# Performance work log

Hardware: AMD Instinct MI355X
Metric: run time of the kernel (lower is better)

The kernel has to match this reference:

```python
import jax, jax.numpy as jnp
import numpy as np

N_NODES = 100000


def _gcn_conv(x, W, b, src, dst, num_nodes):
    # x: [N, Fin] -> h: [N, Fout]
    h = x @ W
    # symmetric normalization deg^-1/2[src] * deg^-1/2[dst] (self-loops already appended)
    ones = jnp.ones(src.shape[0], dtype=x.dtype)
    deg = jax.ops.segment_sum(ones, dst, num_segments=num_nodes)
    dinv = jnp.where(deg > 0, jax.lax.rsqrt(deg), 0.0)
    norm = dinv[src] * dinv[dst]  # [E]
    msg = h[src] * norm[:, None]  # [E, Fout] -- dominant memory traffic
    out = jax.ops.segment_sum(msg, dst, num_segments=num_nodes)
    return out + b


def setup_inputs() -> dict:
    key = jax.random.key(0)
    ks = jax.random.split(key, 8)
    N, F_IN, H = N_NODES, 128, 64
    E = 3200000
    x = jax.random.normal(ks[0], (N, F_IN), dtype=jnp.float32)
    edge_index = jax.random.randint(ks[1], (2, E), 0, N, dtype=jnp.int64)
    s1 = 1.0 / np.sqrt(F_IN)
    s2 = 1.0 / np.sqrt(H)
    return {
        "x": x,
        "edge_index": edge_index,
        "W1": jax.random.normal(ks[2], (F_IN, H), dtype=jnp.float32) * s1,
        "b1": jnp.zeros((H,), dtype=jnp.float32),
        "W2": jax.random.normal(ks[3], (H, H), dtype=jnp.float32) * s2,
        "b2": jnp.zeros((H,), dtype=jnp.float32),
        "W_time": jax.random.normal(ks[4], (H, 1), dtype=jnp.float32) * s2,
        "b_time": jnp.zeros((1,), dtype=jnp.float32),
        "W_event": jax.random.normal(ks[5], (H, 1), dtype=jnp.float32) * s2,
        "b_event": jnp.zeros((1,), dtype=jnp.float32),
    }


def reference(x, edge_index, W1, b1, W2, b2, W_time, b_time, W_event, b_event):
    N = x.shape[0]
    # GCNConv default: add self-loops before normalization/aggregation
    loops = jnp.arange(N, dtype=edge_index.dtype)
    src = jnp.concatenate([edge_index[0], loops])
    dst = jnp.concatenate([edge_index[1], loops])

    h = jax.nn.relu(_gcn_conv(x, W1, b1, src, dst, N))
    # dropout is identity in eval mode
    h = jax.nn.relu(_gcn_conv(h, W2, b2, src, dst, N))

    survival_time = h @ W_time + b_time    # [N, 1]
    event_status = h @ W_event + b_event   # [N, 1]
    return survival_time, event_status
```

## Files before the change

kernel.cpp:

```cpp
#include <hip/hip_runtime.h>
#include <math.h>

constexpr int H = 64;
constexpr int FIN = 128;
constexpr int BIN_SHIFT = 8;
constexpr int BIN_NODES = 1 << BIN_SHIFT;
constexpr int MAX_BINS = 512;
constexpr int BIN_CAP = 10240;
constexpr int SRC_BITS = 24;
constexpr unsigned SRC_MASK = (1u << SRC_BITS) - 1;
constexpr int KB_BLOCKS = 512;
constexpr int KB_ITER = 25;

typedef __attribute__((ext_vector_type(8))) __bf16 bf16x8;
typedef __attribute__((ext_vector_type(4))) float f32x4;

__device__ inline float bf2f(unsigned short u) {
    unsigned v = ((unsigned)u) << 16;
    return __builtin_bit_cast(float, v);
}
__device__ inline unsigned short f2bf(float f) {
    unsigned u = __builtin_bit_cast(unsigned, f);
    unsigned rnd = 0x7FFFu + ((u >> 16) & 1u);
    return (unsigned short)((u + rnd) >> 16);
}

__device__ inline int wave_incl_scan(int v, int lane) {
#pragma unroll
    for (int off = 1; off < 64; off <<= 1) {
        int t = __shfl_up(v, off);
        if (lane >= off) v += t;
    }
    return v;
}

__global__ void k_initcur(int* __restrict__ cursor, int nbins) {
    int i = blockIdx.x * blockDim.x + threadIdx.x;
    if (i < nbins) cursor[i] = i * BIN_CAP;
}

__global__ __launch_bounds__(256) void k_bin(
    const int* __restrict__ src, const int* __restrict__ dst, int E, int nbins,
    int* __restrict__ cursor, int* __restrict__ binned) {
    __shared__ int hist[MAX_BINS];
    __shared__ int base[MAX_BINS];
    int tid = threadIdx.x;
    long long e0 = (long long)E * blockIdx.x / gridDim.x;
    long long e1 = (long long)E * (blockIdx.x + 1) / gridDim.x;
    int chunk = (int)(e1 - e0);
    for (int i = tid; i < nbins; i += 256) hist[i] = 0;
    __syncthreads();
    int packed[KB_ITER];
#pragma unroll
    for (int i = 0; i < KB_ITER; ++i) {
        int o = i * 256 + tid;
        packed[i] = -1;
        if (o < chunk) {
            int d = dst[e0 + o];
            int b = d >> BIN_SHIFT;
            int r = atomicAdd(&hist[b], 1);
            packed[i] = (b << 22) | ((d & (BIN_NODES - 1)) << 14) | r;
        }
    }
    __syncthreads();
    for (int i = tid; i < nbins; i += 256) {
        int h = hist[i];
        base[i] = h ? atomicAdd(&cursor[i], h) : 0;
    }
    __syncthreads();
#pragma unroll
    for (int i = 0; i < KB_ITER; ++i) {
        int o = i * 256 + tid;
        if (o < chunk) {
            unsigned w = (unsigned)packed[i];
            int b = (int)(w >> 22);
            int dl = (int)((w >> 14) & 0xFF);
            int r = (int)(w & 0x3FFF);
            binned[base[b] + r] = (int)(((unsigned)dl << SRC_BITS) | (unsigned)src[e0 + o]);
        }
    }
    for (int o = KB_ITER * 256 + tid; o < chunk; o += 256) {
        int d = dst[e0 + o];
        int b = d >> BIN_SHIFT;
        int r = atomicAdd(&cursor[b], 1);
        binned[r] = (int)(((unsigned)(d & (BIN_NODES - 1)) << SRC_BITS) | (unsigned)src[e0 + o]);
    }
}

__global__ __launch_bounds__(256) void k_binscan(
    const int* __restrict__ cursor, int nbins,
    int* __restrict__ binbase, int* __restrict__ rowptr, int N, int E) {
    __shared__ int wsum[4];
    int tid = threadIdx.x, lane = tid & 63, wid = tid >> 6;
    int b0 = tid * 4;
    int c[4];
#pragma unroll
    for (int k = 0; k < 4; ++k) {
        int b = b0 + k;
        c[k] = (b < nbins) ? cursor[b] - b * BIN_CAP : 0;
    }
    int t = c[0] + c[1] + c[2] + c[3];
    int incl = wave_incl_scan(t, lane);
    if (lane == 63) wsum[wid] = incl;
    __syncthreads();
    int woff = 0;
    for (int w = 0; w < wid; ++w) woff += wsum[w];
    int p = woff + incl - t;
#pragma unroll
    for (int k = 0; k < 4; ++k) {
        int b = b0 + k;
        if (b < nbins) binbase[b] = p;
        p += c[k];
    }
    if (tid == 0) rowptr[N] = E;
}

__global__ __launch_bounds__(256) void k_binsort(
    const int* __restrict__ cursor, const int* __restrict__ binbase,
    const int* __restrict__ binned, int N,
    int* __restrict__ csr_src, int* __restrict__ rowptr, float* __restrict__ dinv) {
    __shared__ int cnt[BIN_NODES];
    __shared__ int excl[BIN_NODES];
    __shared__ int rnk[BIN_NODES];
    __shared__ int wsum[4];
    int bin = blockIdx.x;
    int tid = threadIdx.x, lane = tid & 63, wid = tid >> 6;
    int n = cursor[bin] - bin * BIN_CAP;
    int gbase = binbase[bin];
    const int* bp = binned + (size_t)bin * BIN_CAP;
    cnt[tid] = 0; rnk[tid] = 0;
    __syncthreads();
    for (int i = tid; i < n; i += 256)
        atomicAdd(&cnt[((unsigned)bp[i]) >> SRC_BITS], 1);
    __syncthreads();
    int v = cnt[tid];
    int incl = wave_incl_scan(v, lane);
    if (lane == 63) wsum[wid] = incl;
    __syncthreads();
    int woff = 0;
    for (int w = 0; w < wid; ++w) woff += wsum[w];
    int ex = woff + incl - v;
    excl[tid] = ex;
    int node = bin * BIN_NODES + tid;
    if (node < N) {
        rowptr[node] = gbase + ex;
        dinv[node] = 1.0f / sqrtf((float)v + 1.0f);
    }
    __syncthreads();
    for (int i = tid; i < n; i += 256) {
        unsigned w = (unsigned)bp[i];
        int dl = w >> SRC_BITS;
        int r = atomicAdd(&rnk[dl], 1);
        csr_src[gbase + excl[dl] + r] = (int)(w & SRC_MASK);
    }
}

template<int K, bool RELU_IN>
__global__ __launch_bounds__(256) void k_mgemm(
    const float* __restrict__ X, const float* __restrict__ W,
    const float* __restrict__ bias, const float* __restrict__ dinv,
    int N, unsigned short* __restrict__ A16) {
    constexpr int LDK = K + 8;
    __shared__ short sX[64 * LDK];
    __shared__ short sWt[64 * LDK];
    int tid = threadIdx.x;
    for (int idx = tid; idx < K * 64; idx += 256) {
        int k = idx >> 6, c = idx & 63;
        sWt[c * LDK + k] = (short)f2bf(W[idx]);
    }
    {
        int row = tid >> 2;
        int q0 = (tid & 3) * (K / 4);
        int grow = blockIdx.x * 64 + row;
        const float* xp = X + (size_t)grow * K + q0;
        unsigned* dstp = (unsigned*)&sX[row * LDK + q0];
#pragma unroll
        for (int i = 0; i < K / 16; ++i) {
            float4 v = make_float4(0.f, 0.f, 0.f, 0.f);
            if (grow < N) v = *(const float4*)(xp + i * 4);
            if (RELU_IN) {
                float4 bb = *(const float4*)(bias + q0 + i * 4);
                v.x = fmaxf(v.x + bb.x, 0.f); v.y = fmaxf(v.y + bb.y, 0.f);
                v.z = fmaxf(v.z + bb.z, 0.f); v.w = fmaxf(v.w + bb.w, 0.f);
            }
            unsigned lo = (unsigned)f2bf(v.x) | ((unsigned)f2bf(v.y) << 16);
            unsigned hi = (unsigned)f2bf(v.z) | ((unsigned)f2bf(v.w) << 16);
            dstp[i * 2] = lo;
            dstp[i * 2 + 1] = hi;
        }
    }
    __syncthreads();
    int w = tid >> 6, lane = tid & 63;
    int mrow = lane & 15, kgrp = lane >> 4;
    f32x4 acc[4] = {};
    const short* xbase = &sX[(16 * w + mrow) * LDK + kgrp * 8];
    const short* wbase = &sWt[mrow * LDK + kgrp * 8];
#pragma unroll
    for (int t = 0; t < K / 32; ++t) {
        bf16x8 a = *(const bf16x8*)(xbase + 32 * t);
#pragma unroll
        for (int c = 0; c < 4; ++c) {
            bf16x8 b = *(const bf16x8*)(wbase + 16 * c * LDK + 32 * t);
            acc[c] = __builtin_amdgcn_mfma_f32_16x16x32_bf16(a, b, acc[c], 0, 0, 0);
        }
    }
    int r0g = blockIdx.x * 64 + 16 * w + kgrp * 4;
#pragma unroll
    for (int r = 0; r < 4; ++r) {
        int rg = r0g + r;
        if (rg < N) {
            float dv = dinv[rg];
#pragma unroll
            for (int c = 0; c < 4; ++c)
                A16[(size_t)rg * H + 16 * c + mrow] = f2bf(acc[c][r] * dv);
        }
    }
}

__device__ inline void addbf4(float4& a, ushort4 u) {
    a.x += bf2f(u.x); a.y += bf2f(u.y); a.z += bf2f(u.z); a.w += bf2f(u.w);
}
__device__ inline void add4(float4& a, const float4& b) {
    a.x += b.x; a.y += b.y; a.z += b.z; a.w += b.w;
}

template<bool FUSE>
__global__ __launch_bounds__(256) void k_gather(
    const int* __restrict__ rowptr, const int* __restrict__ csr_src,
    const float* __restrict__ dinv, const unsigned short* __restrict__ A16,
    float* __restrict__ B, int N,
    const float* __restrict__ b2, const float* __restrict__ Wt, const float* __restrict__ bt,
    const float* __restrict__ We, const float* __restrict__ be, float* __restrict__ out) {
    int node = blockIdx.x * 4 + (threadIdx.x >> 6);
    if (node >= N) return;
    int lane = threadIdx.x & 63;
    int grp = lane >> 4, sub = lane & 15;
    const ushort4* A4 = (const ushort4*)A16;
    int beg = rowptr[node], end = rowptr[node + 1];
    float4 a0 = make_float4(0.f, 0.f, 0.f, 0.f), a1 = a0, a2 = a0, a3 = a0;
    if (grp == 0) addbf4(a0, A4[(size_t)node * 16 + sub]);
    for (int e0 = beg; e0 < end; e0 += 64) {
        int m = end - e0; if (m > 64) m = 64;
        int id = (lane < m) ? csr_src[e0 + lane] : 0;
        int c = 0;
        for (; c + 16 <= m; c += 16) {
            int s0 = __shfl(id, c + grp);
            int s1 = __shfl(id, c + 4 + grp);
            int s2 = __shfl(id, c + 8 + grp);
            int s3 = __shfl(id, c + 12 + grp);
            ushort4 v0 = A4[(size_t)s0 * 16 + sub];
            ushort4 v1 = A4[(size_t)s1 * 16 + sub];
            ushort4 v2 = A4[(size_t)s2 * 16 + sub];
            ushort4 v3 = A4[(size_t)s3 * 16 + sub];
            addbf4(a0, v0); addbf4(a1, v1); addbf4(a2, v2); addbf4(a3, v3);
        }
        for (; c < m; c += 4) {
            int cc = c + grp;
            int s = __shfl(id, cc < m ? cc : 0);
            if (cc < m) addbf4(a0, A4[(size_t)s * 16 + sub]);
        }
    }
    add4(a0, a1); add4(a2, a3); add4(a0, a2);
    a0.x += __shfl_xor(a0.x, 16); a0.y += __shfl_xor(a0.y, 16);
    a0.z += __shfl_xor(a0.z, 16); a0.w += __shfl_xor(a0.w, 16);
    a0.x += __shfl_xor(a0.x, 32); a0.y += __shfl_xor(a0.y, 32);
    a0.z += __shfl_xor(a0.z, 32); a0.w += __shfl_xor(a0.w, 32);
    if (grp == 0) {
        float dv = dinv[node];
        a0.x *= dv; a0.y *= dv; a0.z *= dv; a0.w *= dv;
        if (!FUSE) {
            ((float4*)B)[(size_t)node * 16 + sub] = a0;
        } else {
            int f = sub * 4;
            float g0 = fmaxf(a0.x + b2[f + 0], 0.f);
            float g1 = fmaxf(a0.y + b2[f + 1], 0.f);
            float g2 = fmaxf(a0.z + b2[f + 2], 0.f);
            float g3 = fmaxf(a0.w + b2[f + 3], 0.f);
            float p1 = g0 * Wt[f] + g1 * Wt[f + 1] + g2 * Wt[f + 2] + g3 * Wt[f + 3];
            float p2 = g0 * We[f] + g1 * We[f + 1] + g2 * We[f + 2] + g3 * We[f + 3];
#pragma unroll
            for (int off = 1; off < 16; off <<= 1) {
                p1 += __shfl_xor(p1, off);
                p2 += __shfl_xor(p2, off);
            }
            if (sub == 0) {
                out[node] = p1 + bt[0];
                out[N + node] = p2 + be[0];
            }
        }
    }
}

extern "C" void kernel_launch(void* const* d_in, const int* in_sizes, int n_in,
                              void* d_out, int out_size, void* d_ws, size_t ws_size,
                              hipStream_t stream) {
    const float* x  = (const float*)d_in[0];
    const int* edge = (const int*)d_in[1];
    const float* W1 = (const float*)d_in[2];
    const float* b1 = (const float*)d_in[3];
    const float* W2 = (const float*)d_in[4];
    const float* b2 = (const float*)d_in[5];
    const float* Wt = (const float*)d_in[6];
    const float* bt = (const float*)d_in[7];
    const float* We = (const float*)d_in[8];
    const float* be = (const float*)d_in[9];

    int N = in_sizes[0] / FIN;
    int E = in_sizes[1] / 2;
    const int* src = edge;
    const int* dst = edge + E;
    int nbins = (N + BIN_NODES - 1) >> BIN_SHIFT;

    char* ws = (char*)d_ws;
    size_t off = 0;
    auto alloc = [&](size_t bytes) {
        void* p = ws + off;
        off += (bytes + 255) & ~size_t(255);
        return p;
    };
    float* dinv    = (float*)alloc((size_t)N * sizeof(float));
    int*   rowptr  = (int*)alloc((size_t)(N + 1) * sizeof(int));
    int*   cursor  = (int*)alloc((size_t)nbins * sizeof(int));
    int*   binbase = (int*)alloc((size_t)nbins * sizeof(int));
    int*   binned  = (int*)alloc((size_t)nbins * BIN_CAP * sizeof(int));
    int*   csr_src = (int*)alloc((size_t)E * sizeof(int));
    unsigned short* A16 = (unsigned short*)alloc((size_t)N * H * sizeof(unsigned short));
    float* B       = (float*)alloc((size_t)N * H * sizeof(float));

    k_initcur<<<(nbins + 255) / 256, 256, 0, stream>>>(cursor, nbins);
    k_bin<<<KB_BLOCKS, 256, 0, stream>>>(src, dst, E, nbins, cursor, binned);
    k_binscan<<<1, 256, 0, stream>>>(cursor, nbins, binbase, rowptr, N, E);
    k_binsort<<<nbins, 256, 0, stream>>>(cursor, binbase, binned, N, csr_src, rowptr, dinv);

    int ggrid = (N + 63) / 64;
    k_mgemm<FIN, false><<<ggrid, 256, 0, stream>>>(x, W1, nullptr, dinv, N, A16);
    k_gather<false><<<(N + 3) / 4, 256, 0, stream>>>(rowptr, csr_src, dinv, A16, B, N,
                                                     nullptr, nullptr, nullptr, nullptr, nullptr, nullptr);

    k_mgemm<H, true><<<ggrid, 256, 0, stream>>>(B, W2, b1, dinv, N, A16);
    k_gather<true><<<(N + 3) / 4, 256, 0, stream>>>(rowptr, csr_src, dinv, A16, nullptr, N,
                                                    b2, Wt, bt, We, be, (float*)d_out);
}
```

Baseline: 226.3 us.

## Stage binned edges in LDS for coalesced writes; widen gather loads to 16B

The binning kernel now scans its per-block histogram to get local offsets, writes the packed edge words into a shared-memory buffer grouped by bin, then copies each bin's run to global memory with aligned int4 stores, replacing scattered 4-byte writes. The gather kernel has each lane load 16 bytes (8 bf16 features) instead of 8, so 8 lanes cover a row and 8 edges are processed per load step, accumulating with packed float2 adds. This aims to cut scattered-store traffic in binning and the number of load instructions in aggregation, at the cost of about 30KB of extra shared memory per binning block, which may reduce occupancy.

```diff
diff --git a/kernel.cpp b/kernel.cpp
--- a/kernel.cpp
+++ b/kernel.cpp
@@ -14,6 +14,7 @@
 
 typedef __attribute__((ext_vector_type(8))) __bf16 bf16x8;
 typedef __attribute__((ext_vector_type(4))) float f32x4;
+typedef __attribute__((ext_vector_type(2))) float f32x2;
 
 __device__ inline float bf2f(unsigned short u) {
     unsigned v = ((unsigned)u) << 16;
@@ -24,6 +25,8 @@
     unsigned rnd = 0x7FFFu + ((u >> 16) & 1u);
     return (unsigned short)((u + rnd) >> 16);
 }
+__device__ inline float bflo(unsigned u) { return __builtin_bit_cast(float, u << 16); }
+__device__ inline float bfhi(unsigned u) { return __builtin_bit_cast(float, u & 0xFFFF0000u); }
 
 __device__ inline int wave_incl_scan(int v, int lane) {
 #pragma unroll
@@ -44,11 +47,14 @@
     int* __restrict__ cursor, int* __restrict__ binned) {
     __shared__ int hist[MAX_BINS];
     __shared__ int base[MAX_BINS];
-    int tid = threadIdx.x;
+    __shared__ int loff[MAX_BINS];
+    __shared__ int words[KB_ITER * 256];
+    __shared__ int wsum[4];
+    int tid = threadIdx.x, lane = tid & 63, wid = tid >> 6;
     long long e0 = (long long)E * blockIdx.x / gridDim.x;
     long long e1 = (long long)E * (blockIdx.x + 1) / gridDim.x;
     int chunk = (int)(e1 - e0);
-    for (int i = tid; i < nbins; i += 256) hist[i] = 0;
+    for (int i = tid; i < MAX_BINS; i += 256) hist[i] = 0;
     __syncthreads();
     int packed[KB_ITER];
 #pragma unroll
@@ -63,9 +69,20 @@
         }
     }
     __syncthreads();
-    for (int i = tid; i < nbins; i += 256) {
-        int h = hist[i];
-        base[i] = h ? atomicAdd(&cursor[i], h) : 0;
+    {
+        int b0 = tid * 2;
+        int c0 = hist[b0], c1 = hist[b0 + 1];
+        int s = c0 + c1;
+        int incl = wave_incl_scan(s, lane);
+        if (lane == 63) wsum[wid] = incl;
+        __syncthreads();
+        int woff = 0;
+        for (int w = 0; w < wid; ++w) woff += wsum[w];
+        int ex = woff + incl - s;
+        loff[b0] = ex;
+        loff[b0 + 1] = ex + c0;
+        if (b0 < nbins && c0) base[b0] = atomicAdd(&cursor[b0], c0);
+        if (b0 + 1 < nbins && c1) base[b0 + 1] = atomicAdd(&cursor[b0 + 1], c1);
     }
     __syncthreads();
 #pragma unroll
@@ -76,8 +93,22 @@
             int b = (int)(w >> 22);
             int dl = (int)((w >> 14) & 0xFF);
             int r = (int)(w & 0x3FFF);
-            binned[base[b] + r] = (int)(((unsigned)dl << SRC_BITS) | (unsigned)src[e0 + o]);
-        }
+            words[loff[b] + r] = (int)(((unsigned)dl << SRC_BITS) | (unsigned)src[e0 + o]);
+        }
+    }
+    __syncthreads();
+    for (int b = tid; b < nbins; b += 256) {
+        int n = hist[b];
+        if (!n) continue;
+        int g = base[b];
+        int l = loff[b];
+        int i = 0;
+        while (i < n && ((g + i) & 3)) { binned[g + i] = words[l + i]; ++i; }
+        for (; i + 4 <= n; i += 4) {
+            int4 v = make_int4(words[l + i], words[l + i + 1], words[l + i + 2], words[l + i + 3]);
+            *(int4*)&binned[g + i] = v;
+        }
+        for (; i < n; ++i) binned[g + i] = words[l + i];
     }
     for (int o = KB_ITER * 256 + tid; o < chunk; o += 256) {
         int d = dst[e0 + o];
@@ -217,11 +248,12 @@
     }
 }
 
-__device__ inline void addbf4(float4& a, ushort4 u) {
-    a.x += bf2f(u.x); a.y += bf2f(u.y); a.z += bf2f(u.z); a.w += bf2f(u.w);
-}
-__device__ inline void add4(float4& a, const float4& b) {
-    a.x += b.x; a.y += b.y; a.z += b.z; a.w += b.w;
+__device__ inline void acc8(f32x2* acc, uint4 u) {
+    f32x2 v0 = {bflo(u.x), bfhi(u.x)};
+    f32x2 v1 = {bflo(u.y), bfhi(u.y)};
+    f32x2 v2 = {bflo(u.z), bfhi(u.z)};
+    f32x2 v3 = {bflo(u.w), bfhi(u.w)};
+    acc[0] += v0; acc[1] += v1; acc[2] += v2; acc[3] += v3;
 }
 
 template<bool FUSE>
@@ -234,52 +266,60 @@
     int node = blockIdx.x * 4 + (threadIdx.x >> 6);
     if (node >= N) return;
     int lane = threadIdx.x & 63;
-    int grp = lane >> 4, sub = lane & 15;
-    const ushort4* A4 = (const ushort4*)A16;
+    int grp = lane >> 3, sub = lane & 7;
+    const uint4* A8 = (const uint4*)A16;
     int beg = rowptr[node], end = rowptr[node + 1];
-    float4 a0 = make_float4(0.f, 0.f, 0.f, 0.f), a1 = a0, a2 = a0, a3 = a0;
-    if (grp == 0) addbf4(a0, A4[(size_t)node * 16 + sub]);
+    f32x2 acc[4] = {};
+    f32x2 acc2[4] = {};
+    if (grp == 0) acc8(acc, A8[(size_t)node * 8 + sub]);
     for (int e0 = beg; e0 < end; e0 += 64) {
         int m = end - e0; if (m > 64) m = 64;
         int id = (lane < m) ? csr_src[e0 + lane] : 0;
         int c = 0;
         for (; c + 16 <= m; c += 16) {
             int s0 = __shfl(id, c + grp);
-            int s1 = __shfl(id, c + 4 + grp);
-            int s2 = __shfl(id, c + 8 + grp);
-            int s3 = __shfl(id, c + 12 + grp);
-            ushort4 v0 = A4[(size_t)s0 * 16 + sub];
-            ushort4 v1 = A4[(size_t)s1 * 16 + sub];
-            ushort4 v2 = A4[(size_t)s2 * 16 + sub];
-            ushort4 v3 = A4[(size_t)s3 * 16 + sub];
-            addbf4(a0, v0); addbf4(a1, v1); addbf4(a2, v2); addbf4(a3, v3);
-        }
-        for (; c < m; c += 4) {
+            int s1 = __shfl(id, c + 8 + grp);
+            uint4 u0 = A8[(size_t)s0 * 8 + sub];
+            uint4 u1 = A8[(size_t)s1 * 8 + sub];
+            acc8(acc, u0);
+            acc8(acc2, u1);
+        }
+        for (; c < m; c += 8) {
             int cc = c + grp;
             int s = __shfl(id, cc < m ? cc : 0);
-            if (cc < m) addbf4(a0, A4[(size_t)s * 16 + sub]);
-        }
-    }
-    add4(a0, a1); add4(a2, a3); add4(a0, a2);
-    a0.x += __shfl_xor(a0.x, 16); a0.y += __shfl_xor(a0.y, 16);
-    a0.z += __shfl_xor(a0.z, 16); a0.w += __shfl_xor(a0.w, 16);
-    a0.x += __shfl_xor(a0.x, 32); a0.y += __shfl_xor(a0.y, 32);
-    a0.z += __shfl_xor(a0.z, 32); a0.w += __shfl_xor(a0.w, 32);
+            if (cc < m) acc8(acc, A8[(size_t)s * 8 + sub]);
+        }
+    }
+#pragma unroll
+    for (int j = 0; j < 4; ++j) acc[j] += acc2[j];
+#pragma unroll
+    for (int off = 8; off < 64; off <<= 1) {
+#pragma unroll
+        for (int j = 0; j < 4; ++j) {
+            acc[j][0] += __shfl_xor(acc[j][0], off);
+            acc[j][1] += __shfl_xor(acc[j][1], off);
+        }
+    }
     if (grp == 0) {
         float dv = dinv[node];
-        a0.x *= dv; a0.y *= dv; a0.z *= dv; a0.w *= dv;
+        float r[8];
+#pragma unroll
+        for (int j = 0; j < 4; ++j) { r[2 * j] = acc[j][0] * dv; r[2 * j + 1] = acc[j][1] * dv; }
         if (!FUSE) {
-            ((float4*)B)[(size_t)node * 16 + sub] = a0;
+            float* bp = B + (size_t)node * H + sub * 8;
+            *(float4*)bp = make_float4(r[0], r[1], r[2], r[3]);
+            *(float4*)(bp + 4) = make_float4(r[4], r[5], r[6], r[7]);
         } else {
-            int f = sub * 4;
-            float g0 = fmaxf(a0.x + b2[f + 0], 0.f);
-            float g1 = fmaxf(a0.y + b2[f + 1], 0.f);
-            float g2 = fmaxf(a0.z + b2[f + 2], 0.f);
-            float g3 = fmaxf(a0.w + b2[f + 3], 0.f);
-            float p1 = g0 * Wt[f] + g1 * Wt[f + 1] + g2 * Wt[f + 2] + g3 * Wt[f + 3];
-            float p2 = g0 * We[f] + g1 * We[f + 1] + g2 * We[f + 2] + g3 * We[f + 3];
-#pragma unroll
-            for (int off = 1; off < 16; off <<= 1) {
+            int f = sub * 8;
+            float p1 = 0.f, p2 = 0.f;
+#pragma unroll
+            for (int j = 0; j < 8; ++j) {
+                float g = fmaxf(r[j] + b2[f + j], 0.f);
+                p1 += g * Wt[f + j];
+                p2 += g * We[f + j];
+            }
+#pragma unroll
+            for (int off = 1; off < 8; off <<= 1) {
                 p1 += __shfl_xor(p1, off);
                 p2 += __shfl_xor(p2, off);
             }
```

New measurement: 232.8 us. 1.03x slower.
